# Kernel optimization log

Hardware: AMD Instinct MI355X
Metric: run time of the kernel (lower is better)

Reference implementation:

```python
import jax, jax.numpy as jnp
import numpy as np

WS = 7       # window size
SHIFT = 3    # shift size
NH = 6       # num heads

def layernorm(x, w, b, eps=1e-5):
    mu = jnp.mean(x, axis=-1, keepdims=True)
    var = jnp.var(x, axis=-1, keepdims=True)
    return (x - mu) * jax.lax.rsqrt(var + eps) * w + b

def setup_inputs() -> dict:
    key = jax.random.key(0)
    ks = jax.random.split(key, 8)
    B, H, W, C = 16, 56, 56, 192
    hid = 4 * C
    s = lambda k, shape, fan: jax.random.normal(k, shape, jnp.float32) * (fan ** -0.5)
    return {
        "x": jax.random.normal(ks[0], (B, H, W, C), jnp.float32),
        "ln1_w": jnp.ones((C,), jnp.float32), "ln1_b": jnp.zeros((C,), jnp.float32),
        "qkv_w": s(ks[1], (C, 3 * C), C), "qkv_b": jnp.zeros((3 * C,), jnp.float32),
        "proj_w": s(ks[2], (C, C), C), "proj_b": jnp.zeros((C,), jnp.float32),
        "ln2_w": jnp.ones((C,), jnp.float32), "ln2_b": jnp.zeros((C,), jnp.float32),
        "mlp_w1": s(ks[3], (C, hid), C), "mlp_b1": jnp.zeros((hid,), jnp.float32),
        "mlp_w2": s(ks[4], (hid, C), hid), "mlp_b2": jnp.zeros((C,), jnp.float32),
    }

def reference(x, ln1_w, ln1_b, qkv_w, qkv_b, proj_w, proj_b, ln2_w, ln2_b, mlp_w1, mlp_b1, mlp_w2, mlp_b2):
    B, H, W, C = x.shape
    hd = C // NH
    scale = hd ** -0.5
    N = WS * WS

    shortcut = x
    xn = layernorm(x, ln1_w, ln1_b)
    # cyclic shift
    xs = jnp.roll(xn, shift=(-SHIFT, -SHIFT), axis=(1, 2))
    # window partition: [B*nW, N, C]
    xw = xs.reshape(B, H // WS, WS, W // WS, WS, C)
    xw = xw.transpose(0, 1, 3, 2, 4, 5).reshape(-1, N, C)

    # window attention
    qkv = xw @ qkv_w + qkv_b                       # [Bn, N, 3C]
    qkv = qkv.reshape(-1, N, 3, NH, hd).transpose(2, 0, 3, 1, 4)  # [3, Bn, NH, N, hd]
    q, k, v = qkv[0], qkv[1], qkv[2]
    attn = jnp.einsum('bhqd,bhkd->bhqk', q, k) * scale
    attn = jax.nn.softmax(attn, axis=-1)
    o = jnp.einsum('bhqk,bhkd->bhqd', attn, v)     # [Bn, NH, N, hd]
    o = o.transpose(0, 2, 1, 3).reshape(-1, N, C)
    o = o @ proj_w + proj_b

    # window reverse
    o = o.reshape(B, H // WS, W // WS, WS, WS, C)
    o = o.transpose(0, 1, 3, 2, 4, 5).reshape(B, H, W, C)
    # reverse shift
    o = jnp.roll(o, shift=(SHIFT, SHIFT), axis=(1, 2))

    x = shortcut + o
    # MLP (exact GELU, matching torch nn.GELU default)
    h = layernorm(x, ln2_w, ln2_b)
    h = jax.nn.gelu(h @ mlp_w1 + mlp_b1, approximate=False)
    x = x + (h @ mlp_w2 + mlp_b2)
    return x
```

## Files before the change

kernel.cpp:

```cpp
#include <hip/hip_runtime.h>
#include <hip/hip_bf16.h>
#include <math.h>

typedef __attribute__((ext_vector_type(8))) short short8;
typedef __attribute__((ext_vector_type(4))) float float4v;

#define C_DIM 192
#define NHEADS 6
#define NTOK 50176

__device__ __forceinline__ float bf2f(unsigned short u){
  union { unsigned int i; float f; } x; x.i = ((unsigned int)u) << 16; return x.f;
}
__device__ __forceinline__ unsigned short f2bf(float f){
  union { float f; unsigned int i; } x; x.f = f;
  unsigned int r = x.i + 0x7fff + ((x.i >> 16) & 1);
  return (unsigned short)(r >> 16);
}

__device__ __forceinline__ void gload_lds16(const unsigned short* g, unsigned short* l){
  __builtin_amdgcn_global_load_lds((const __attribute__((address_space(1))) void*)g,
                                   (__attribute__((address_space(3))) void*)l, 16, 0, 0);
}

__device__ __forceinline__ int nat_token(int r){
  int win = r / 49, n = r - win * 49;
  int b = win >> 6, rem = win & 63;
  int hs = (rem >> 3) * 7 + n / 7;
  int ws = (rem & 7) * 7 + n % 7;
  int h = hs + 3; if (h >= 56) h -= 56;
  int w = ws + 3; if (w >= 56) w -= 56;
  return (b * 56 + h) * 56 + w;
}

__device__ __forceinline__ float gelu_f(float v){
  float z2 = v * (1.5957691216057308f + 0.07135481282553456f * v * v);
  z2 = fminf(z2, 30.f);
  float p = __expf(z2);
  return v * (p / (p + 1.f));
}

__global__ void transpose_kernel(const float* __restrict__ in,
                                 unsigned short* __restrict__ out, int R, int Cc){
  int idx = blockIdx.x * 256 + threadIdx.x;
  if (idx < R * Cc){ int r = idx / Cc, c = idx - r * Cc; out[(long)c * R + r] = f2bf(in[idx]); }
}

__global__ __launch_bounds__(256) void ln1_kernel(const float* __restrict__ x,
                                                  const float* __restrict__ w,
                                                  const float* __restrict__ b,
                                                  unsigned short* __restrict__ out){
  int wave = threadIdx.x >> 6, lane = threadIdx.x & 63;
  int r = blockIdx.x * 4 + wave;
  int src = nat_token(r);
  const float* xp = x + (long)src * C_DIM;
  float v0 = xp[lane], v1 = xp[lane + 64], v2 = xp[lane + 128];
  float s = v0 + v1 + v2, s2 = v0*v0 + v1*v1 + v2*v2;
  for (int m = 32; m >= 1; m >>= 1){ s += __shfl_xor(s, m, 64); s2 += __shfl_xor(s2, m, 64); }
  float mean = s * (1.f/192.f);
  float var  = s2 * (1.f/192.f) - mean*mean;
  float rs = rsqrtf(var + 1e-5f);
  unsigned short* op = out + (long)r * C_DIM;
  op[lane]       = f2bf((v0-mean)*rs*w[lane]       + b[lane]);
  op[lane + 64]  = f2bf((v1-mean)*rs*w[lane + 64]  + b[lane + 64]);
  op[lane + 128] = f2bf((v2-mean)*rs*w[lane + 128] + b[lane + 128]);
}

__global__ __launch_bounds__(256) void ln2_kernel(const float* __restrict__ y,
                                                  const float* __restrict__ w,
                                                  const float* __restrict__ b,
                                                  unsigned short* __restrict__ out){
  int wave = threadIdx.x >> 6, lane = threadIdx.x & 63;
  int r = blockIdx.x * 4 + wave;
  const float* yp = y + (long)r * C_DIM;
  float v0 = yp[lane], v1 = yp[lane + 64], v2 = yp[lane + 128];
  float s = v0 + v1 + v2, s2 = v0*v0 + v1*v1 + v2*v2;
  for (int m = 32; m >= 1; m >>= 1){ s += __shfl_xor(s, m, 64); s2 += __shfl_xor(s2, m, 64); }
  float mean = s * (1.f/192.f);
  float var  = s2 * (1.f/192.f) - mean*mean;
  float rs = rsqrtf(var + 1e-5f);
  unsigned short* op = out + (long)r * C_DIM;
  op[lane]       = f2bf((v0-mean)*rs*w[lane]       + b[lane]);
  op[lane + 64]  = f2bf((v1-mean)*rs*w[lane + 64]  + b[lane + 64]);
  op[lane + 128] = f2bf((v2-mean)*rs*w[lane + 128] + b[lane + 128]);
}

__global__ __launch_bounds__(256) void attn_kernel(const unsigned short* __restrict__ qkv,
                                                   unsigned short* __restrict__ o){
  __shared__ unsigned short pbuf[4][64][72];
  int wave = threadIdx.x >> 6, lane = threadIdx.x & 63;
  int quad = lane >> 4, l16 = lane & 15;
  int wid = blockIdx.x * 4 + wave;
  int win = wid / NHEADS, head = wid - win * NHEADS;
  const unsigned short* qp = qkv + (long)win * 49 * 576 + head * 32;
  const unsigned short* kp = qp + 192;
  const unsigned short* vp = qp + 384;

  short8 qa[4], kb[4];
  #pragma unroll
  for (int mi = 0; mi < 4; mi++){
    int m = mi * 16 + l16; if (m > 48) m = 48;
    qa[mi] = *(const short8*)&qp[(long)m * 576 + quad * 8];
  }
  #pragma unroll
  for (int ni = 0; ni < 4; ni++){
    int n = ni * 16 + l16; if (n > 48) n = 48;
    kb[ni] = *(const short8*)&kp[(long)n * 576 + quad * 8];
  }
  float4v S[4][4];
  #pragma unroll
  for (int mi = 0; mi < 4; mi++)
    #pragma unroll
    for (int ni = 0; ni < 4; ni++) S[mi][ni] = (float4v)0.f;
  #pragma unroll
  for (int mi = 0; mi < 4; mi++)
    #pragma unroll
    for (int ni = 0; ni < 4; ni++)
      S[mi][ni] = __builtin_amdgcn_mfma_f32_16x16x32_bf16(qa[mi], kb[ni], S[mi][ni], 0, 0, 0);

  #pragma unroll
  for (int mi = 0; mi < 4; mi++){
    #pragma unroll
    for (int r = 0; r < 4; r++){
      float e[4];
      float sum = 0.f;
      #pragma unroll
      for (int ni = 0; ni < 4; ni++){
        int n = ni * 16 + l16;
        float s = S[mi][ni][r] * 0.17677669529663687f;
        s = fminf(s, 80.f);
        float ev = (n <= 48) ? __expf(s) : 0.f;
        e[ni] = ev; sum += ev;
      }
      sum += __shfl_xor(sum, 1, 64);
      sum += __shfl_xor(sum, 2, 64);
      sum += __shfl_xor(sum, 4, 64);
      sum += __shfl_xor(sum, 8, 64);
      float inv = 1.f / sum;
      int m = mi * 16 + quad * 4 + r;
      #pragma unroll
      for (int ni = 0; ni < 4; ni++)
        pbuf[wave][m][ni * 16 + l16] = f2bf(e[ni] * inv);
    }
  }
  __syncthreads();

  short8 vb[2][2];
  #pragma unroll
  for (int kk2 = 0; kk2 < 2; kk2++){
    #pragma unroll
    for (int ni = 0; ni < 2; ni++){
      union { unsigned short us[8]; short8 v8; } u;
      #pragma unroll
      for (int j = 0; j < 8; j++){
        int k = kk2 * 32 + quad * 8 + j; if (k > 48) k = 48;
        u.us[j] = vp[(long)k * 576 + ni * 16 + l16];
      }
      vb[kk2][ni] = u.v8;
    }
  }

  float4v O[4][2];
  #pragma unroll
  for (int mi = 0; mi < 4; mi++)
    #pragma unroll
    for (int ni = 0; ni < 2; ni++) O[mi][ni] = (float4v)0.f;
  #pragma unroll
  for (int kk2 = 0; kk2 < 2; kk2++){
    short8 pa[4];
    #pragma unroll
    for (int mi = 0; mi < 4; mi++)
      pa[mi] = *(const short8*)&pbuf[wave][mi * 16 + l16][kk2 * 32 + quad * 8];
    #pragma unroll
    for (int mi = 0; mi < 4; mi++)
      #pragma unroll
      for (int ni = 0; ni < 2; ni++)
        O[mi][ni] = __builtin_amdgcn_mfma_f32_16x16x32_bf16(pa[mi], vb[kk2][ni], O[mi][ni], 0, 0, 0);
  }

  #pragma unroll
  for (int mi = 0; mi < 4; mi++){
    int m0 = mi * 16 + quad * 4;
    #pragma unroll
    for (int r = 0; r < 4; r++){
      if (m0 + r <= 48){
        #pragma unroll
        for (int ni = 0; ni < 2; ni++)
          o[((long)win * 49 + m0 + r) * C_DIM + head * 32 + ni * 16 + l16] = f2bf(O[mi][ni][r]);
      }
    }
  }
}

template<int EPI>
__global__ __launch_bounds__(256) void gemm_kernel(const unsigned short* __restrict__ A,
                                                   const unsigned short* __restrict__ Bt,
                                                   const float* __restrict__ bias,
                                                   unsigned short* __restrict__ Cout,
                                                   float* __restrict__ Fout,
                                                   const float* __restrict__ Xres,
                                                   int N, int K){
  __shared__ unsigned short As[128 * 64];
  __shared__ unsigned short Bs[64 * 64];
  int tid = threadIdx.x;
  int wave = tid >> 6, lane = tid & 63, quad = lane >> 4, l16 = lane & 15;
  int wm = (wave >> 1) * 64, wn = (wave & 1) * 32;
  int lrow = lane >> 3, lg = lane & 7;
  int gcol = (lg ^ lrow) * 8;
  float4v acc[4][2];
  #pragma unroll
  for (int i = 0; i < 4; i++)
    #pragma unroll
    for (int jj = 0; jj < 2; jj++) acc[i][jj] = (float4v)0.f;

  long arow0 = (long)blockIdx.x * 128;
  long brow0 = (long)blockIdx.y * 64;
  int sw = (l16 & 7);

  for (int k0 = 0; k0 < K; k0 += 64){
    #pragma unroll
    for (int t = 0; t < 4; t++){
      int ci = wave + 4 * t;
      gload_lds16(&A[(arow0 + ci * 8 + lrow) * (long)K + k0 + gcol], &As[ci * 512]);
    }
    #pragma unroll
    for (int t = 0; t < 2; t++){
      int ci = wave + 4 * t;
      gload_lds16(&Bt[(brow0 + ci * 8 + lrow) * (long)K + k0 + gcol], &Bs[ci * 512]);
    }
    __syncthreads();
    #pragma unroll
    for (int kk8 = 0; kk8 < 8; kk8 += 4){
      short8 a[4], b[2];
      #pragma unroll
      for (int mi = 0; mi < 4; mi++)
        a[mi] = *(const short8*)&As[(wm + mi*16 + l16) * 64 + ((quad + kk8) ^ sw) * 8];
      #pragma unroll
      for (int ni = 0; ni < 2; ni++)
        b[ni] = *(const short8*)&Bs[(wn + ni*16 + l16) * 64 + ((quad + kk8) ^ sw) * 8];
      #pragma unroll
      for (int mi = 0; mi < 4; mi++)
        #pragma unroll
        for (int ni = 0; ni < 2; ni++)
          acc[mi][ni] = __builtin_amdgcn_mfma_f32_16x16x32_bf16(a[mi], b[ni], acc[mi][ni], 0, 0, 0);
    }
    __syncthreads();
  }

  #pragma unroll
  for (int mi = 0; mi < 4; mi++){
    #pragma unroll
    for (int reg = 0; reg < 4; reg++){
      long r = arow0 + wm + mi*16 + quad*4 + reg;
      #pragma unroll
      for (int ni = 0; ni < 2; ni++){
        int c = (int)(brow0 + wn + ni*16 + l16);
        float v = acc[mi][ni][reg] + bias[c];
        if (EPI == 0){
          Cout[r * N + c] = f2bf(v);
        } else {
          int t = nat_token((int)r);
          long idx = (long)t * C_DIM + c;
          Fout[idx] = Xres[idx] + v;
        }
      }
    }
  }
}

__global__ __launch_bounds__(256, 2) void fused_mlp_kernel(const unsigned short* __restrict__ hn,
                                                           const unsigned short* __restrict__ w1t,
                                                           const float* __restrict__ b1,
                                                           const unsigned short* __restrict__ w2t,
                                                           const float* __restrict__ b2,
                                                           float* __restrict__ y){
  __shared__ __attribute__((aligned(16))) unsigned short As[3 * 64 * 64];
  __shared__ __attribute__((aligned(16))) unsigned short Bs[192 * 64];
  __shared__ __attribute__((aligned(16))) unsigned short Hs[64 * 72];
  int tid = threadIdx.x;
  int wave = tid >> 6, lane = tid & 63, quad = lane >> 4, l16 = lane & 15;
  int lrow = lane >> 3, lg = lane & 7;
  int gcol = (lg ^ lrow) * 8;
  int sw = l16 & 7;
  int wrow0 = wave * 16;
  long arow0 = (long)blockIdx.x * 64;

  float4v acc[12];
  #pragma unroll
  for (int i = 0; i < 12; i++) acc[i] = (float4v)0.f;

  #pragma unroll
  for (int t = 0; t < 6; t++){
    int i = wave + 4 * t; int gg = i >> 3, br8 = (i & 7) << 3;
    gload_lds16(&hn[(arow0 + br8 + lrow) * C_DIM + gg * 64 + gcol], &As[gg * 4096 + br8 * 64]);
  }
  #pragma unroll
  for (int t = 0; t < 6; t++){
    int i = wave + 4 * t; int gg = i >> 3, br8 = (i & 7) << 3;
    gload_lds16(&w1t[(br8 + lrow) * 192 + gg * 64 + gcol], &Bs[gg * 4096 + br8 * 64]);
  }
  __syncthreads();

  #pragma unroll 1
  for (int j = 0; j < 12; j++){
    float4v s[4];
    #pragma unroll
    for (int ni = 0; ni < 4; ni++) s[ni] = (float4v)0.f;
    #pragma unroll
    for (int kk = 0; kk < 6; kk++){
      int gg = kk >> 1, xb = (kk & 1) * 4;
      short8 a = *(const short8*)&As[gg * 4096 + (wrow0 + l16) * 64 + ((xb + quad) ^ sw) * 8];
      #pragma unroll
      for (int ni = 0; ni < 4; ni++){
        short8 b = *(const short8*)&Bs[gg * 4096 + (ni * 16 + l16) * 64 + ((xb + quad) ^ sw) * 8];
        s[ni] = __builtin_amdgcn_mfma_f32_16x16x32_bf16(a, b, s[ni], 0, 0, 0);
      }
    }
    #pragma unroll
    for (int ni = 0; ni < 4; ni++){
      float bb = b1[j * 64 + ni * 16 + l16];
      #pragma unroll
      for (int r = 0; r < 4; r++){
        float g = gelu_f(s[ni][r] + bb);
        Hs[(wrow0 + quad * 4 + r) * 72 + ni * 16 + l16] = f2bf(g);
      }
    }
    __syncthreads();

    #pragma unroll
    for (int t = 0; t < 6; t++){
      int i = wave + 4 * t; int br8 = i << 3;
      gload_lds16(&w2t[(br8 + lrow) * 768 + j * 64 + gcol], &Bs[br8 * 64]);
    }
    __syncthreads();

    #pragma unroll
    for (int kk = 0; kk < 2; kk++){
      short8 pa = *(const short8*)&Hs[(wrow0 + l16) * 72 + kk * 32 + quad * 8];
      #pragma unroll
      for (int ni = 0; ni < 12; ni++){
        short8 b = *(const short8*)&Bs[(ni * 16 + l16) * 64 + ((kk * 4 + quad) ^ sw) * 8];
        acc[ni] = __builtin_amdgcn_mfma_f32_16x16x32_bf16(pa, b, acc[ni], 0, 0, 0);
      }
    }
    __syncthreads();

    if (j < 11){
      #pragma unroll
      for (int t = 0; t < 6; t++){
        int i = wave + 4 * t; int gg = i >> 3, br8 = (i & 7) << 3;
        gload_lds16(&w1t[((j + 1) * 64 + br8 + lrow) * 192 + gg * 64 + gcol],
                    &Bs[gg * 4096 + br8 * 64]);
      }
      __syncthreads();
    }
  }

  #pragma unroll
  for (int ni = 0; ni < 12; ni++){
    int c = ni * 16 + l16;
    float bb = b2[c];
    #pragma unroll
    for (int r = 0; r < 4; r++){
      long row = arow0 + wrow0 + quad * 4 + r;
      long idx = row * C_DIM + c;
      y[idx] = y[idx] + acc[ni][r] + bb;
    }
  }
}

extern "C" void kernel_launch(void* const* d_in, const int* in_sizes, int n_in,
                              void* d_out, int out_size, void* d_ws, size_t ws_size,
                              hipStream_t stream){
  const float* x      = (const float*)d_in[0];
  const float* ln1_w  = (const float*)d_in[1];
  const float* ln1_b  = (const float*)d_in[2];
  const float* qkv_w  = (const float*)d_in[3];
  const float* qkv_b  = (const float*)d_in[4];
  const float* proj_w = (const float*)d_in[5];
  const float* proj_b = (const float*)d_in[6];
  const float* ln2_w  = (const float*)d_in[7];
  const float* ln2_b  = (const float*)d_in[8];
  const float* mlp_w1 = (const float*)d_in[9];
  const float* mlp_b1 = (const float*)d_in[10];
  const float* mlp_w2 = (const float*)d_in[11];
  const float* mlp_b2 = (const float*)d_in[12];
  float* out = (float*)d_out;

  char* ws = (char*)d_ws;
  unsigned short* qkv_wt = (unsigned short*)(ws);
  unsigned short* proj_wt= (unsigned short*)(ws + 221184);
  unsigned short* w1t    = (unsigned short*)(ws + 294912);
  unsigned short* w2t    = (unsigned short*)(ws + 589824);
  unsigned short* R1     = (unsigned short*)(ws + 884736);
  unsigned short* R0     = (unsigned short*)(ws + 20152320);

  unsigned short* xw   = R1;
  unsigned short* obuf = R1;
  unsigned short* hn   = R1;
  unsigned short* qkv  = R0;

  transpose_kernel<<<(110592 + 255) / 256, 256, 0, stream>>>(qkv_w, qkv_wt, 192, 576);
  transpose_kernel<<<(36864  + 255) / 256, 256, 0, stream>>>(proj_w, proj_wt, 192, 192);
  transpose_kernel<<<(147456 + 255) / 256, 256, 0, stream>>>(mlp_w1, w1t, 192, 768);
  transpose_kernel<<<(147456 + 255) / 256, 256, 0, stream>>>(mlp_w2, w2t, 768, 192);

  ln1_kernel<<<NTOK / 4, 256, 0, stream>>>(x, ln1_w, ln1_b, xw);
  gemm_kernel<0><<<dim3(392, 9),  256, 0, stream>>>(xw, qkv_wt, qkv_b, qkv, nullptr, nullptr, 576, 192);
  attn_kernel<<<(NTOK / 49) * NHEADS / 4, 256, 0, stream>>>(qkv, obuf);
  gemm_kernel<1><<<dim3(392, 3),  256, 0, stream>>>(obuf, proj_wt, proj_b, nullptr, out, x, 192, 192);
  ln2_kernel<<<NTOK / 4, 256, 0, stream>>>(out, ln2_w, ln2_b, hn);
  fused_mlp_kernel<<<NTOK / 64, 256, 0, stream>>>(hn, w1t, mlp_b1, w2t, mlp_b2, out);
}
```

Before: 281.1 us.

## Double-buffer W1/W2 tiles in fused MLP with 32-wide hidden chunks

The fused MLP loop now walks the hidden dimension in 32-column chunks instead of 64. Both the W1 and W2 slices for chunk j+1 are prefetched into a second LDS buffer while chunk j is computed, which cuts each iteration from four block barriers to one. The GELU intermediate stays within each wave's own rows, so the second GEMM can start without a block-wide sync. The trade-offs are more LDS use (about 77KB per block against an occupancy target of two blocks per CU) and half as many MFMAs per iteration.

```diff
diff --git a/kernel.cpp b/kernel.cpp
--- a/kernel.cpp
+++ b/kernel.cpp
@@ -275,13 +275,16 @@
                                                            const float* __restrict__ b2,
                                                            float* __restrict__ y){
   __shared__ __attribute__((aligned(16))) unsigned short As[3 * 64 * 64];
-  __shared__ __attribute__((aligned(16))) unsigned short Bs[192 * 64];
-  __shared__ __attribute__((aligned(16))) unsigned short Hs[64 * 72];
+  __shared__ __attribute__((aligned(16))) unsigned short W1[2][3 * 32 * 64];
+  __shared__ __attribute__((aligned(16))) unsigned short W2[2][192 * 32];
+  __shared__ __attribute__((aligned(16))) unsigned short Hs[64 * 40];
   int tid = threadIdx.x;
   int wave = tid >> 6, lane = tid & 63, quad = lane >> 4, l16 = lane & 15;
   int lrow = lane >> 3, lg = lane & 7;
   int gcol = (lg ^ lrow) * 8;
   int sw = l16 & 7;
+  int w2_r = lane >> 2, w2_pg = lane & 3;
+  int w2_g = w2_pg ^ (w2_r & 3);
   int wrow0 = wave * 16;
   long arow0 = (long)blockIdx.x * 64;
 
@@ -295,64 +298,58 @@
     gload_lds16(&hn[(arow0 + br8 + lrow) * C_DIM + gg * 64 + gcol], &As[gg * 4096 + br8 * 64]);
   }
   #pragma unroll
-  for (int t = 0; t < 6; t++){
-    int i = wave + 4 * t; int gg = i >> 3, br8 = (i & 7) << 3;
-    gload_lds16(&w1t[(br8 + lrow) * 192 + gg * 64 + gcol], &Bs[gg * 4096 + br8 * 64]);
-  }
-  __syncthreads();
+  for (int t = 0; t < 3; t++){
+    int i = wave + 4 * t;
+    int gg = i >> 2, br8 = (i & 3) << 3;
+    gload_lds16(&w1t[(br8 + lrow) * C_DIM + gg * 64 + gcol], &W1[0][gg * 2048 + br8 * 64]);
+    gload_lds16(&w2t[((long)(i * 16 + w2_r)) * 768 + w2_g * 8], &W2[0][i * 512]);
+  }
 
   #pragma unroll 1
-  for (int j = 0; j < 12; j++){
-    float4v s[4];
-    #pragma unroll
-    for (int ni = 0; ni < 4; ni++) s[ni] = (float4v)0.f;
+  for (int j = 0; j < 24; j++){
+    __syncthreads();
+    if (j < 23){
+      int nb = (j + 1) & 1;
+      int col0 = (j + 1) * 32;
+      #pragma unroll
+      for (int t = 0; t < 3; t++){
+        int i = wave + 4 * t;
+        int gg = i >> 2, br8 = (i & 3) << 3;
+        gload_lds16(&w1t[(col0 + br8 + lrow) * C_DIM + gg * 64 + gcol],
+                    &W1[nb][gg * 2048 + br8 * 64]);
+        gload_lds16(&w2t[((long)(i * 16 + w2_r)) * 768 + col0 + w2_g * 8],
+                    &W2[nb][i * 512]);
+      }
+    }
+    int cb = j & 1;
+
+    float4v s[2];
+    s[0] = (float4v)0.f; s[1] = (float4v)0.f;
     #pragma unroll
     for (int kk = 0; kk < 6; kk++){
       int gg = kk >> 1, xb = (kk & 1) * 4;
       short8 a = *(const short8*)&As[gg * 4096 + (wrow0 + l16) * 64 + ((xb + quad) ^ sw) * 8];
       #pragma unroll
-      for (int ni = 0; ni < 4; ni++){
-        short8 b = *(const short8*)&Bs[gg * 4096 + (ni * 16 + l16) * 64 + ((xb + quad) ^ sw) * 8];
-        s[ni] = __builtin_amdgcn_mfma_f32_16x16x32_bf16(a, b, s[ni], 0, 0, 0);
-      }
-    }
-    #pragma unroll
-    for (int ni = 0; ni < 4; ni++){
-      float bb = b1[j * 64 + ni * 16 + l16];
+      for (int ti = 0; ti < 2; ti++){
+        short8 b = *(const short8*)&W1[cb][gg * 2048 + (ti * 16 + l16) * 64 + ((xb + quad) ^ sw) * 8];
+        s[ti] = __builtin_amdgcn_mfma_f32_16x16x32_bf16(a, b, s[ti], 0, 0, 0);
+      }
+    }
+    #pragma unroll
+    for (int ti = 0; ti < 2; ti++){
+      float bb = b1[j * 32 + ti * 16 + l16];
       #pragma unroll
       for (int r = 0; r < 4; r++){
-        float g = gelu_f(s[ni][r] + bb);
-        Hs[(wrow0 + quad * 4 + r) * 72 + ni * 16 + l16] = f2bf(g);
-      }
-    }
-    __syncthreads();
-
-    #pragma unroll
-    for (int t = 0; t < 6; t++){
-      int i = wave + 4 * t; int br8 = i << 3;
-      gload_lds16(&w2t[(br8 + lrow) * 768 + j * 64 + gcol], &Bs[br8 * 64]);
-    }
-    __syncthreads();
-
-    #pragma unroll
-    for (int kk = 0; kk < 2; kk++){
-      short8 pa = *(const short8*)&Hs[(wrow0 + l16) * 72 + kk * 32 + quad * 8];
-      #pragma unroll
-      for (int ni = 0; ni < 12; ni++){
-        short8 b = *(const short8*)&Bs[(ni * 16 + l16) * 64 + ((kk * 4 + quad) ^ sw) * 8];
-        acc[ni] = __builtin_amdgcn_mfma_f32_16x16x32_bf16(pa, b, acc[ni], 0, 0, 0);
-      }
-    }
-    __syncthreads();
-
-    if (j < 11){
-      #pragma unroll
-      for (int t = 0; t < 6; t++){
-        int i = wave + 4 * t; int gg = i >> 3, br8 = (i & 7) << 3;
-        gload_lds16(&w1t[((j + 1) * 64 + br8 + lrow) * 192 + gg * 64 + gcol],
-                    &Bs[gg * 4096 + br8 * 64]);
-      }
-      __syncthreads();
+        float g = gelu_f(s[ti][r] + bb);
+        Hs[(wrow0 + quad * 4 + r) * 40 + ti * 16 + l16] = f2bf(g);
+      }
+    }
+    short8 pa = *(const short8*)&Hs[(wrow0 + l16) * 40 + quad * 8];
+    #pragma unroll
+    for (int ni = 0; ni < 12; ni++){
+      int row = ni * 16 + l16;
+      short8 b = *(const short8*)&W2[cb][row * 32 + ((quad ^ (row & 3)) * 8)];
+      acc[ni] = __builtin_amdgcn_mfma_f32_16x16x32_bf16(pa, b, acc[ni], 0, 0, 0);
     }
   }
 
```

Result: slower. 296.8 us (+5.6%).
